# Kernel tuning notes

Hardware: AMD Instinct MI355X
Metric: run time of the kernel (lower is better)

Reference implementation:

```python
import jax, jax.numpy as jnp
import numpy as np

N_NODES = 100000
N_EDGES = 3200000
# (out_dim, in_dim) for the 4 BayesianLinear layers: mlp1 = [5->16, 16->32], mlp2 = [35->16, 16->1]
LAYER_DIMS = [(16, 5), (32, 16), (16, 35), (1, 16)]


def setup_inputs() -> dict:
    key = jax.random.key(0)
    ks = iter(jax.random.split(key, 32))
    inp = {}
    inp["x"] = jax.random.normal(next(ks), (N_NODES, 3), jnp.float32)
    inp["edge_attr"] = jax.random.normal(next(ks), (N_EDGES, 2), jnp.float32)
    inp["edge_index"] = jax.random.randint(next(ks), (2, N_EDGES), 0, N_NODES, dtype=jnp.int64)
    for li, (o, i) in enumerate(LAYER_DIMS, 1):
        inp[f"l{li}_wmu"] = jax.random.normal(next(ks), (o, i), jnp.float32) * 0.1
        inp[f"l{li}_wrho"] = jax.random.normal(next(ks), (o, i), jnp.float32) * 0.1 - 5.0
        inp[f"l{li}_bmu"] = jax.random.normal(next(ks), (o,), jnp.float32) * 0.1
        inp[f"l{li}_brho"] = jax.random.normal(next(ks), (o,), jnp.float32) * 0.1 - 5.0
        inp[f"l{li}_eps_w"] = jax.random.normal(next(ks), (o, i), jnp.float32)
        inp[f"l{li}_eps_b"] = jax.random.normal(next(ks), (o,), jnp.float32)
    return inp


def _bayes_linear(h, wmu, wrho, bmu, brho, eps_w, eps_b):
    # sampled weight: W = mu + softplus(rho) * eps  (blitz BayesianLinear)
    W = wmu + jax.nn.softplus(wrho) * eps_w          # [out, in]
    b = bmu + jax.nn.softplus(brho) * eps_b          # [out]
    return h @ W.T + b


def _igconv(x, edge_index, edge_attr, p1, p2, p3, p4):
    src, dst = edge_index[0], edge_index[1]          # x_j = x[src], aggregate at dst
    x_j = x[src]                                     # [E, 3] irregular gather
    m = jnp.concatenate([x_j, edge_attr], axis=1)    # [E, 5]
    m = jax.nn.relu(_bayes_linear(m, *p1))           # [E, 16]
    m = jax.nn.relu(_bayes_linear(m, *p2))           # [E, 32]
    agg = jax.ops.segment_max(m, dst, num_segments=x.shape[0])  # [N, 32]
    agg = jnp.where(jnp.isneginf(agg), 0.0, agg)     # nodes with no in-edges -> 0
    h = jnp.concatenate([x, agg], axis=1)            # [N, 35]
    h = jax.nn.relu(_bayes_linear(h, *p3))           # [N, 16]
    comb = jax.nn.sigmoid(_bayes_linear(h, *p4))     # [N, 1]
    return jnp.concatenate([x[:, :2], comb], axis=1) # [N, 3]


def reference(x, edge_attr, edge_index,
              l1_wmu, l1_wrho, l1_bmu, l1_brho, l1_eps_w, l1_eps_b,
              l2_wmu, l2_wrho, l2_bmu, l2_brho, l2_eps_w, l2_eps_b,
              l3_wmu, l3_wrho, l3_bmu, l3_brho, l3_eps_w, l3_eps_b,
              l4_wmu, l4_wrho, l4_bmu, l4_brho, l4_eps_w, l4_eps_b):
    p1 = (l1_wmu, l1_wrho, l1_bmu, l1_brho, l1_eps_w, l1_eps_b)
    p2 = (l2_wmu, l2_wrho, l2_bmu, l2_brho, l2_eps_w, l2_eps_b)
    p3 = (l3_wmu, l3_wrho, l3_bmu, l3_brho, l3_eps_w, l3_eps_b)
    p4 = (l4_wmu, l4_wrho, l4_bmu, l4_brho, l4_eps_w, l4_eps_b)
    h = x
    for _ in range(3):  # three stacked applications of the same IGConv
        h = _igconv(h, edge_index, edge_attr, p1, p2, p3, p4)
    return h
```

## Files before the change

kernel.cpp:

```cpp
#include <hip/hip_runtime.h>
#include <math.h>

#define WTOT  1233
#define PKOFS 1280
#define PKTOT 352

#define SCAT_CAP 12288

typedef __fp16 h2 __attribute__((ext_vector_type(2)));
typedef __fp16 f16x8 __attribute__((ext_vector_type(8)));
typedef float f32x16 __attribute__((ext_vector_type(16)));

__device__ __forceinline__ h2 u2h(unsigned int u) { return __builtin_bit_cast(h2, u); }
__device__ __forceinline__ unsigned int h2u(h2 h) { return __builtin_bit_cast(unsigned int, h); }
#define DOT2(a, b, c) __builtin_amdgcn_fdot2((a), (b), (c), false)

__device__ __forceinline__ float softplus_f(float x) {
  return fmaxf(x, 0.f) + log1pf(expf(-fabsf(x)));
}

struct PrepArgs {
  const float* wmu[4]; const float* wrho[4]; const float* epsw[4];
  const float* bmu[4]; const float* brho[4]; const float* epsb[4];
  float* out; int* bucketCur; int* etot; int nbuck;
};

__global__ void prep_all_kernel(PrepArgs a) {
  const int wsz[4] = {80, 512, 560, 16};
  const int wof[4] = {0, 96, 640, 1216};
  const int bsz[4] = {16, 32, 16, 1};
  const int bof[4] = {80, 608, 1200, 1232};
  float* wg = a.out;
  int tid = threadIdx.x;
  if (tid < a.nbuck) a.bucketCur[tid] = 0;
  if (tid == 1023) *a.etot = 0;
#pragma unroll
  for (int l = 0; l < 4; l++) {
    for (int i = tid; i < wsz[l]; i += 1024)
      wg[wof[l] + i] = a.wmu[l][i] + softplus_f(a.wrho[l][i]) * a.epsw[l][i];
    for (int i = tid; i < bsz[l]; i += 1024)
      wg[bof[l] + i] = a.bmu[l][i] + softplus_f(a.brho[l][i]) * a.epsb[l][i];
  }
  __syncthreads();
  unsigned int* wp = (unsigned int*)(wg + PKOFS);
  int t = tid;
  if (t < 16) {
    wp[t]      = h2u(h2{(__fp16)wg[t * 5 + 0], (__fp16)wg[t * 5 + 1]});
    wp[16 + t] = h2u(h2{(__fp16)wg[t * 5 + 2], (__fp16)0.f});
    wp[32 + t] = h2u(h2{(__fp16)wg[t * 5 + 3], (__fp16)wg[t * 5 + 4]});
    ((float*)wp)[304 + t] = wg[80 + t];
  }
  if (t < 32) {
    ((float*)wp)[320 + t] = wg[608 + t];
    for (int j = 0; j < 8; j++)
      wp[48 + t * 8 + j] =
          h2u(h2{(__fp16)wg[96 + t * 16 + 2 * j], (__fp16)wg[96 + t * 16 + 2 * j + 1]});
  }
}

__global__ __launch_bounds__(1024) void bhist_kernel(
    const int* __restrict__ dst, int* __restrict__ bucketCur,
    const float* __restrict__ x, uint2* __restrict__ xpk,
    unsigned int* __restrict__ agg32, int E, int N, int NBUCK) {
  __shared__ int h[1024];
  int tid = threadIdx.x;
  for (int i = tid; i < NBUCK; i += 1024) h[i] = 0;
  int nbase = blockIdx.x * 256;
  if (tid < 256) {
    int i = nbase + tid;
    if (i < N) {
      h2 a = __builtin_amdgcn_cvt_pkrtz(x[3 * i], x[3 * i + 1]);
      h2 b = __builtin_amdgcn_cvt_pkrtz(x[3 * i + 2], 0.f);
      xpk[i] = make_uint2(h2u(a), h2u(b));
    }
  }
  {
    uint4 z = make_uint4(0u, 0u, 0u, 0u);
    uint4* ap = (uint4*)agg32;
    size_t lim = ((size_t)N + 1) * 8;
    size_t i0 = (size_t)nbase * 8 + tid;
    if (i0 < lim) ap[i0] = z;
    size_t i1 = i0 + 1024;
    if (i1 < (size_t)(nbase + 256) * 8 && i1 < lim) ap[i1] = z;
  }
  __syncthreads();
  int base = blockIdx.x * 8192;
#pragma unroll
  for (int r = 0; r < 2; r++) {
    int e = base + r * 4096 + tid * 4;
    if (e + 3 < E) {
      int4 d4v = *(const int4*)(dst + e);
      atomicAdd(&h[d4v.x >> 8], 1);
      atomicAdd(&h[d4v.y >> 8], 1);
      atomicAdd(&h[d4v.z >> 8], 1);
      atomicAdd(&h[d4v.w >> 8], 1);
    } else {
      for (int k = 0; k < 4; k++)
        if (e + k < E) atomicAdd(&h[dst[e + k] >> 8], 1);
    }
  }
  __syncthreads();
  for (int i = tid; i < NBUCK; i += 1024) {
    int c = h[i];
    if (c) atomicAdd(&bucketCur[i], c);
  }
}

__global__ __launch_bounds__(1024) void scanBk_kernel(int* __restrict__ bucketCur,
                                                      int* __restrict__ bucketOff,
                                                      int NBUCK) {
  __shared__ int wsum[16];
  __shared__ int woff[16];
  int tid = threadIdx.x, lane = tid & 63, wid = tid >> 6;
  int v = (tid < NBUCK) ? bucketCur[tid] : 0;
  int x = v;
#pragma unroll
  for (int off = 1; off < 64; off <<= 1) {
    int t = __shfl_up(x, off, 64);
    if (lane >= off) x += t;
  }
  if (lane == 63) wsum[wid] = x;
  __syncthreads();
  if (wid == 0) {
    int s = (lane < 16) ? wsum[lane] : 0;
#pragma unroll
    for (int off = 1; off < 16; off <<= 1) {
      int t = __shfl_up(s, off, 64);
      if (lane >= off) s += t;
    }
    if (lane < 16) woff[lane] = s - wsum[lane];
  }
  __syncthreads();
  int excl = woff[wid] + x - v;
  if (tid < NBUCK) {
    bucketOff[tid] = excl;
    bucketCur[tid] = excl;
    if (tid == NBUCK - 1) bucketOff[NBUCK] = excl + v;
  }
}

__global__ __launch_bounds__(1024) void part_kernel(
    const int* __restrict__ src, const int* __restrict__ dst,
    const float2* __restrict__ ea, int* __restrict__ bucketCur,
    uint2* __restrict__ brec8, int E, int NBUCK) {
  __shared__ int h[1024];
  int tid = threadIdx.x;
  for (int i = tid; i < NBUCK; i += 1024) h[i] = 0;
  __syncthreads();
  int base = blockIdx.x * 8192;
  int d[8], s[8];
  unsigned int a[8];
  bool v[8];
#pragma unroll
  for (int j = 0; j < 8; j++) {
    int e = base + j * 1024 + tid;
    v[j] = e < E;
    if (v[j]) {
      d[j] = dst[e];
      s[j] = src[e];
      float2 t = ea[e];
      a[j] = h2u(__builtin_amdgcn_cvt_pkrtz(t.x, t.y));
      atomicAdd(&h[d[j] >> 8], 1);
    }
  }
  __syncthreads();
  for (int i = tid; i < NBUCK; i += 1024) {
    int c = h[i];
    h[i] = c ? atomicAdd(&bucketCur[i], c) : 0;
  }
  __syncthreads();
#pragma unroll
  for (int j = 0; j < 8; j++) {
    if (v[j]) {
      int pos = atomicAdd(&h[d[j] >> 8], 1);
      brec8[pos] = make_uint2(a[j], (unsigned int)s[j] | ((unsigned int)(d[j] & 255) << 24));
    }
  }
}

__global__ __launch_bounds__(1024) void scat_kernel(
    const uint2* __restrict__ brec8, const int* __restrict__ bucketOff,
    int* __restrict__ etot, uint2* __restrict__ se8, unsigned int* __restrict__ d4,
    int N) {
  __shared__ int cnt[256];
  __shared__ int sstart[256];
  __shared__ int wsum[4];
  __shared__ int woff[4];
  __shared__ int sbase;
  __shared__ int ptot;
  __shared__ __align__(16) uint2 stage[SCAT_CAP];
  __shared__ unsigned int staged4[SCAT_CAP / 4];
  int b = blockIdx.x, tid = threadIdx.x;
  int lane = tid & 63, wid = tid >> 6;
  if (tid < 256) cnt[tid] = 0;
  __syncthreads();
  int e0 = bucketOff[b], e1 = bucketOff[b + 1];
  for (int i = e0 + tid; i < e1; i += 1024) atomicAdd(&cnt[brec8[i].y >> 24], 1);
  __syncthreads();
  int v = 0;
  if (tid < 256) v = (cnt[tid] + 3) & ~3;
  int x = v;
#pragma unroll
  for (int off = 1; off < 64; off <<= 1) {
    int t = __shfl_up(x, off, 64);
    if (lane >= off) x += t;
  }
  if (tid < 256 && lane == 63) wsum[wid] = x;
  __syncthreads();
  if (wid == 0 && lane < 4) {
    int s = wsum[lane];
#pragma unroll
    for (int off = 1; off < 4; off <<= 1) {
      int t = __shfl_up(s, off, 64);
      if (lane >= off) s += t;
    }
    woff[lane] = s - wsum[lane];
    if (lane == 3) { ptot = s; sbase = atomicAdd(etot, s); }
  }
  __syncthreads();
  int total = ptot;
  if (total <= SCAT_CAP) {
    if (tid < 256) {
      int start = woff[wid] + x - v;
      sstart[tid] = start;
      cnt[tid] = start;
    }
    __syncthreads();
    for (int i = e0 + tid; i < e1; i += 1024) {
      uint2 t = brec8[i];
      int pos = atomicAdd(&cnt[t.y >> 24], 1);
      stage[pos] = make_uint2(t.y & 0x00FFFFFFu, t.x);
    }
    __syncthreads();
    if (tid < 256) {
      int start = sstart[tid];
      int endR = cnt[tid];
      int endP = start + ((endR - start + 3) & ~3);
      if (endR > start) {
        uint2 rep = stage[start];
        for (int k = endR; k < endP; k++) stage[k] = rep;
        unsigned int node = (unsigned int)(b * 256 + tid);
        for (int k = start; k < endP; k += 4) staged4[k >> 2] = node;
      }
    }
    __syncthreads();
    int base = sbase;
    uint4* dstp = (uint4*)(se8 + base);
    const uint4* srcp = (const uint4*)stage;
    int n4 = total >> 1;
    for (int i = tid; i < n4; i += 1024) dstp[i] = srcp[i];
    unsigned int* d4p = d4 + (base >> 2);
    int nd = total >> 2;
    for (int i = tid; i < nd; i += 1024) d4p[i] = staged4[i];
  } else {
    if (tid < 256) {
      int start = sbase + woff[wid] + x - v;
      sstart[tid] = start;
      cnt[tid] = start;
    }
    __syncthreads();
    for (int i = e0 + tid; i < e1; i += 1024) {
      uint2 t = brec8[i];
      int pos = atomicAdd(&cnt[t.y >> 24], 1);
      se8[pos] = make_uint2(t.y & 0x00FFFFFFu, t.x);
    }
    __syncthreads();
    if (tid < 256) {
      int node = b * 256 + tid;
      int start = sstart[tid];
      int endR = cnt[tid];
      int endP = start + ((endR - start + 3) & ~3);
      if (endR > start) {
        uint2 rep = se8[start];
        for (int k = endR; k < endP; k++) se8[k] = rep;
        for (int k = start; k < endP; k += 4) d4[k >> 2] = (unsigned int)node;
      }
    }
  }
}

__global__ __launch_bounds__(256) void edge_kernel(
    const uint2* __restrict__ xpk, const uint2* __restrict__ se8,
    const unsigned int* __restrict__ d4, unsigned int* __restrict__ agg32,
    const float* __restrict__ wg, const int* __restrict__ pEtot,
    unsigned int tag, int N) {
  __shared__ __align__(16) unsigned int lds[4][64][12];
  const unsigned int* wp = (const unsigned int*)(wg + PKOFS);
  const float* bf = (const float*)wp;
  const int Etot = *pEtot;
  if (blockIdx.x * 256 >= Etot) return;
  const int tid = threadIdx.x;
  const int lane = tid & 63;
  const int wslot = tid >> 6;
  const int e = blockIdx.x * 256 + tid;

  bool vld = e < Etot;
  uint2 se = vld ? se8[e] : make_uint2(0u, 0u);
  int d = vld ? (int)d4[e >> 2] : N;
  uint2 xs = xpk[se.x];

  h2 p01 = u2h(xs.x), p2v = u2h(xs.y), pea = u2h(se.y);
  unsigned int m1[8];
#pragma unroll
  for (int p = 0; p < 8; p++) {
    const int oA = 2 * p, oB = 2 * p + 1;
    float sA = DOT2(p01, u2h(wp[oA]),
                DOT2(p2v, u2h(wp[16 + oA]),
                DOT2(pea, u2h(wp[32 + oA]), bf[304 + oA])));
    float sB = DOT2(p01, u2h(wp[oB]),
                DOT2(p2v, u2h(wp[16 + oB]),
                DOT2(pea, u2h(wp[32 + oB]), bf[304 + oB])));
    m1[p] = h2u(__builtin_amdgcn_cvt_pkrtz(fmaxf(sA, 0.f), fmaxf(sB, 0.f)));
  }

  uint4* rowp = (uint4*)&lds[wslot][lane][0];
  rowp[0] = make_uint4(m1[0], m1[1], m1[2], m1[3]);
  rowp[1] = make_uint4(m1[4], m1[5], m1[6], m1[7]);
  asm volatile("s_waitcnt lgkmcnt(0)" ::: "memory");
  __builtin_amdgcn_sched_barrier(0);

  const int col = lane & 31;
  const int h = lane >> 5;
  f16x8 bfrag = __builtin_bit_cast(f16x8, *(const uint4*)&wp[48 + col * 8 + 4 * h]);
  float bias = bf[320 + col];
  f32x16 cini;
#pragma unroll
  for (int i = 0; i < 16; i++) cini[i] = bias;

  __builtin_amdgcn_s_setprio(1);
  f16x8 a0 = __builtin_bit_cast(f16x8, *(const uint4*)&lds[wslot][col][4 * h]);
  f16x8 a1 = __builtin_bit_cast(f16x8, *(const uint4*)&lds[wslot][32 + col][4 * h]);
  f32x16 acc0 = __builtin_amdgcn_mfma_f32_32x32x16_f16(a0, bfrag, cini, 0, 0, 0);
  f32x16 acc1 = __builtin_amdgcn_mfma_f32_32x32x16_f16(a1, bfrag, cini, 0, 0, 0);

  float bm[2][4];
#pragma unroll
  for (int q = 0; q < 4; q++) {
    bm[0][q] = fmaxf(fmaxf(acc0[4 * q], acc0[4 * q + 1]),
                     fmaxf(acc0[4 * q + 2], fmaxf(acc0[4 * q + 3], 0.f)));
    bm[1][q] = fmaxf(fmaxf(acc1[4 * q], acc1[4 * q + 1]),
                     fmaxf(acc1[4 * q + 2], fmaxf(acc1[4 * q + 3], 0.f)));
  }
  __builtin_amdgcn_s_setprio(0);

  int dp4 = __shfl_up(d, 4, 64);
  bool isHead = ((lane & 3) == 0) && (lane == 0 || d != dp4);
  unsigned long long hm = __ballot(isHead);

  unsigned long long rem = hm;
  while (rem) {
    int a = (int)__builtin_ctzll(rem);
    rem &= rem - 1;
    int b = rem ? (int)__builtin_ctzll(rem) : 64;
    int rd = __shfl(d, a, 64);
    int A = a >> 2, B = b >> 2;
    float mx = 0.f;
#pragma unroll
    for (int g = 0; g < 2; g++) {
#pragma unroll
      for (int q = 0; q < 4; q++) {
        int blk = 8 * g + 2 * q + h;
        bool in = (blk >= A) && (blk < B);
        mx = fmaxf(mx, in ? bm[g][q] : 0.f);
      }
    }
    mx = fmaxf(mx, __shfl_xor(mx, 32, 64));
    if (lane < 32 && rd < N) {
      unsigned int bits = __float_as_uint(mx);
      atomicMax(agg32 + (size_t)rd * 32 + col, (tag << 30) | (bits >> 1));
    }
  }
}

__global__ __launch_bounds__(256) void node_kernel(
    const float* __restrict__ x, const float* __restrict__ cin,
    float* __restrict__ cout, uint2* __restrict__ xpk,
    float* __restrict__ outFinal, const unsigned int* __restrict__ agg32,
    const float* __restrict__ wg, unsigned int tag, int n) {
  int nid = blockIdx.x * blockDim.x + threadIdx.x;
  if (nid >= n) return;
  const uint4* ap = (const uint4*)(agg32 + (size_t)nid * 32);
  uint4 q[8];
#pragma unroll
  for (int i = 0; i < 8; i++) q[i] = ap[i];
  float av[32];
#pragma unroll
  for (int i = 0; i < 8; i++) {
    unsigned int w[4] = {q[i].x, q[i].y, q[i].z, q[i].w};
#pragma unroll
    for (int j = 0; j < 4; j++) {
      unsigned int u = ((w[j] >> 30) == tag) ? ((w[j] & 0x3FFFFFFFu) << 1) : 0u;
      av[4 * i + j] = __uint_as_float(u);
    }
  }
  float x0 = x[3 * nid], x1 = x[3 * nid + 1];
  float x2 = cin ? cin[nid] : x[3 * nid + 2];
  float h[16];
#pragma unroll
  for (int o = 0; o < 16; o++) {
    float sa = wg[1200 + o];
    sa = fmaf(wg[640 + o * 35 + 0], x0, sa);
    sa = fmaf(wg[640 + o * 35 + 1], x1, sa);
    sa = fmaf(wg[640 + o * 35 + 2], x2, sa);
#pragma unroll
    for (int k = 0; k < 32; k++) sa = fmaf(wg[640 + o * 35 + 3 + k], av[k], sa);
    h[o] = fmaxf(sa, 0.f);
  }
  float z4 = wg[1232];
#pragma unroll
  for (int k = 0; k < 16; k++) z4 = fmaf(wg[1216 + k], h[k], z4);
  float comb = 1.f / (1.f + expf(-z4));
  cout[nid] = comb;
  ((unsigned int*)xpk)[2 * nid + 1] = h2u(__builtin_amdgcn_cvt_pkrtz(comb, 0.f));
  if (outFinal) {
    outFinal[3 * nid] = x0;
    outFinal[3 * nid + 1] = x1;
    outFinal[3 * nid + 2] = comb;
  }
}

extern "C" void kernel_launch(void* const* d_in, const int* in_sizes, int n_in,
                              void* d_out, int out_size, void* d_ws, size_t ws_size,
                              hipStream_t stream) {
  const float* x = (const float*)d_in[0];
  const float* ea = (const float*)d_in[1];
  const int* eidx = (const int*)d_in[2];
  const int N = in_sizes[0] / 3;
  const int E = in_sizes[1] / 2;
  const int* src = eidx;
  const int* dst = eidx + E;
  const int NBUCK = (N + 255) >> 8;
  const int EP = E + 3 * N;

  char* p = (char*)d_ws;
  size_t off = 0;
  auto alloc = [&](size_t bytes) -> char* {
    char* r = p + off;
    off = (off + bytes + 255) & ~(size_t)255;
    return r;
  };
  float* wbuf = (float*)alloc((size_t)(PKOFS + PKTOT) * 4);
  int* bucketOff = (int*)alloc(((size_t)NBUCK + 1) * 4);
  int* bucketCur = (int*)alloc((size_t)NBUCK * 4);
  int* etot = (int*)alloc(4);
  uint2* se8 = (uint2*)alloc((size_t)EP * 8);
  unsigned int* d4 = (unsigned int*)alloc(((size_t)(EP + 3) / 4 + 1) * 4);
  unsigned int* agg32 = (unsigned int*)alloc(((size_t)N + 1) * 32 * 4);
  uint2* xpk = (uint2*)alloc((size_t)N * 8);
  char* uni = alloc((size_t)E * 8);
  uint2* brec8 = (uint2*)uni;
  float* bufA = (float*)uni;
  float* bufB = (float*)(uni + (((size_t)N * 4 + 255) & ~(size_t)255));
  (void)ws_size;

  PrepArgs pa;
  for (int l = 0; l < 4; l++) {
    pa.wmu[l] = (const float*)d_in[3 + 6 * l + 0];
    pa.wrho[l] = (const float*)d_in[3 + 6 * l + 1];
    pa.bmu[l] = (const float*)d_in[3 + 6 * l + 2];
    pa.brho[l] = (const float*)d_in[3 + 6 * l + 3];
    pa.epsw[l] = (const float*)d_in[3 + 6 * l + 4];
    pa.epsb[l] = (const float*)d_in[3 + 6 * l + 5];
  }
  pa.out = wbuf;
  pa.bucketCur = bucketCur;
  pa.etot = etot;
  pa.nbuck = NBUCK;

  const int TB = 256;
  auto blocks = [&](int n) { return dim3((n + TB - 1) / TB); };

  prep_all_kernel<<<dim3(1), dim3(1024), 0, stream>>>(pa);
  {
    int gb = (E + 8191) / 8192;
    int gn = (N + 255) / 256;
    int g = gb > gn ? gb : gn;
    bhist_kernel<<<dim3(g), dim3(1024), 0, stream>>>(dst, bucketCur, x, xpk, agg32,
                                                     E, N, NBUCK);
  }
  scanBk_kernel<<<dim3(1), dim3(1024), 0, stream>>>(bucketCur, bucketOff, NBUCK);
  part_kernel<<<dim3((E + 8191) / 8192), dim3(1024), 0, stream>>>(
      src, dst, (const float2*)ea, bucketCur, brec8, E, NBUCK);
  scat_kernel<<<dim3(NBUCK), dim3(1024), 0, stream>>>(brec8, bucketOff, etot, se8, d4, N);

  float* outp = (float*)d_out;
  const int ebp = (EP + 255) / 256;
  edge_kernel<<<dim3(ebp), dim3(TB), 0, stream>>>(xpk, se8, d4, agg32, wbuf, etot, 1u, N);
  node_kernel<<<blocks(N), dim3(TB), 0, stream>>>(x, nullptr, bufA, xpk, nullptr,
                                                  agg32, wbuf, 1u, N);
  edge_kernel<<<dim3(ebp), dim3(TB), 0, stream>>>(xpk, se8, d4, agg32, wbuf, etot, 2u, N);
  node_kernel<<<blocks(N), dim3(TB), 0, stream>>>(x, bufA, bufB, xpk, nullptr,
                                                  agg32, wbuf, 2u, N);
  edge_kernel<<<dim3(ebp), dim3(TB), 0, stream>>>(xpk, se8, d4, agg32, wbuf, etot, 3u, N);
  node_kernel<<<blocks(N), dim3(TB), 0, stream>>>(x, bufB, bufA, xpk, outp,
                                                  agg32, wbuf, 3u, N);
}
```

Measured before the change: 326.4 us.

## Make edge kernel persistent grid-stride per wave with prefetch of next edge tile

Caps the edge kernel grid at 2048 blocks and has each wave loop over 64-edge tiles in a grid-stride fashion. While it processes the current tile it prefetches the next tile's sorted edge records and destination indices. Per-wave setup such as the B fragment and bias is loaded once and reused across tiles. This aims to cut launch and block overhead and hide load latency, at the cost of extra registers and possibly less latency hiding from oversubscription.

```diff
diff --git a/kernel.cpp b/kernel.cpp
--- a/kernel.cpp
+++ b/kernel.cpp
@@ -266,14 +266,14 @@
     }
     __syncthreads();
     if (tid < 256) {
-      int node = b * 256 + tid;
+      unsigned int node = (unsigned int)(b * 256 + tid);
       int start = sstart[tid];
       int endR = cnt[tid];
       int endP = start + ((endR - start + 3) & ~3);
       if (endR > start) {
         uint2 rep = se8[start];
         for (int k = endR; k < endP; k++) se8[k] = rep;
-        for (int k = start; k < endP; k += 4) d4[k >> 2] = (unsigned int)node;
+        for (int k = start; k < endP; k += 4) d4[k >> 2] = node;
       }
     }
   }
@@ -283,41 +283,16 @@
     const uint2* __restrict__ xpk, const uint2* __restrict__ se8,
     const unsigned int* __restrict__ d4, unsigned int* __restrict__ agg32,
     const float* __restrict__ wg, const int* __restrict__ pEtot,
-    unsigned int tag, int N) {
+    unsigned int tag, int N, int nwv) {
   __shared__ __align__(16) unsigned int lds[4][64][12];
   const unsigned int* wp = (const unsigned int*)(wg + PKOFS);
   const float* bf = (const float*)wp;
   const int Etot = *pEtot;
-  if (blockIdx.x * 256 >= Etot) return;
   const int tid = threadIdx.x;
   const int lane = tid & 63;
   const int wslot = tid >> 6;
-  const int e = blockIdx.x * 256 + tid;
-
-  bool vld = e < Etot;
-  uint2 se = vld ? se8[e] : make_uint2(0u, 0u);
-  int d = vld ? (int)d4[e >> 2] : N;
-  uint2 xs = xpk[se.x];
-
-  h2 p01 = u2h(xs.x), p2v = u2h(xs.y), pea = u2h(se.y);
-  unsigned int m1[8];
-#pragma unroll
-  for (int p = 0; p < 8; p++) {
-    const int oA = 2 * p, oB = 2 * p + 1;
-    float sA = DOT2(p01, u2h(wp[oA]),
-                DOT2(p2v, u2h(wp[16 + oA]),
-                DOT2(pea, u2h(wp[32 + oA]), bf[304 + oA])));
-    float sB = DOT2(p01, u2h(wp[oB]),
-                DOT2(p2v, u2h(wp[16 + oB]),
-                DOT2(pea, u2h(wp[32 + oB]), bf[304 + oB])));
-    m1[p] = h2u(__builtin_amdgcn_cvt_pkrtz(fmaxf(sA, 0.f), fmaxf(sB, 0.f)));
-  }
-
-  uint4* rowp = (uint4*)&lds[wslot][lane][0];
-  rowp[0] = make_uint4(m1[0], m1[1], m1[2], m1[3]);
-  rowp[1] = make_uint4(m1[4], m1[5], m1[6], m1[7]);
-  asm volatile("s_waitcnt lgkmcnt(0)" ::: "memory");
-  __builtin_amdgcn_sched_barrier(0);
+  int w = blockIdx.x * 4 + wslot;
+  if (w * 64 >= Etot) return;
 
   const int col = lane & 31;
   const int h = lane >> 5;
@@ -327,48 +302,93 @@
 #pragma unroll
   for (int i = 0; i < 16; i++) cini[i] = bias;
 
-  __builtin_amdgcn_s_setprio(1);
-  f16x8 a0 = __builtin_bit_cast(f16x8, *(const uint4*)&lds[wslot][col][4 * h]);
-  f16x8 a1 = __builtin_bit_cast(f16x8, *(const uint4*)&lds[wslot][32 + col][4 * h]);
-  f32x16 acc0 = __builtin_amdgcn_mfma_f32_32x32x16_f16(a0, bfrag, cini, 0, 0, 0);
-  f32x16 acc1 = __builtin_amdgcn_mfma_f32_32x32x16_f16(a1, bfrag, cini, 0, 0, 0);
-
-  float bm[2][4];
-#pragma unroll
-  for (int q = 0; q < 4; q++) {
-    bm[0][q] = fmaxf(fmaxf(acc0[4 * q], acc0[4 * q + 1]),
-                     fmaxf(acc0[4 * q + 2], fmaxf(acc0[4 * q + 3], 0.f)));
-    bm[1][q] = fmaxf(fmaxf(acc1[4 * q], acc1[4 * q + 1]),
-                     fmaxf(acc1[4 * q + 2], fmaxf(acc1[4 * q + 3], 0.f)));
-  }
-  __builtin_amdgcn_s_setprio(0);
-
-  int dp4 = __shfl_up(d, 4, 64);
-  bool isHead = ((lane & 3) == 0) && (lane == 0 || d != dp4);
-  unsigned long long hm = __ballot(isHead);
-
-  unsigned long long rem = hm;
-  while (rem) {
-    int a = (int)__builtin_ctzll(rem);
-    rem &= rem - 1;
-    int b = rem ? (int)__builtin_ctzll(rem) : 64;
-    int rd = __shfl(d, a, 64);
-    int A = a >> 2, B = b >> 2;
-    float mx = 0.f;
-#pragma unroll
-    for (int g = 0; g < 2; g++) {
-#pragma unroll
-      for (int q = 0; q < 4; q++) {
-        int blk = 8 * g + 2 * q + h;
-        bool in = (blk >= A) && (blk < B);
-        mx = fmaxf(mx, in ? bm[g][q] : 0.f);
+  int e = w * 64 + lane;
+  uint2 seC = (e < Etot) ? se8[e] : make_uint2(0u, 0u);
+  int dC = (e < Etot) ? (int)d4[e >> 2] : N;
+
+  while (true) {
+    int wn = w + nwv;
+    bool hasNext = (wn * 64 < Etot);
+    uint2 seN = make_uint2(0u, 0u);
+    int dN = N;
+    if (hasNext) {
+      int en = wn * 64 + lane;
+      if (en < Etot) {
+        seN = se8[en];
+        dN = (int)d4[en >> 2];
       }
     }
-    mx = fmaxf(mx, __shfl_xor(mx, 32, 64));
-    if (lane < 32 && rd < N) {
-      unsigned int bits = __float_as_uint(mx);
-      atomicMax(agg32 + (size_t)rd * 32 + col, (tag << 30) | (bits >> 1));
-    }
+
+    uint2 xs = xpk[seC.x];
+    h2 p01 = u2h(xs.x), p2v = u2h(xs.y), pea = u2h(seC.y);
+    unsigned int m1[8];
+#pragma unroll
+    for (int p = 0; p < 8; p++) {
+      const int oA = 2 * p, oB = 2 * p + 1;
+      float sA = DOT2(p01, u2h(wp[oA]),
+                  DOT2(p2v, u2h(wp[16 + oA]),
+                  DOT2(pea, u2h(wp[32 + oA]), bf[304 + oA])));
+      float sB = DOT2(p01, u2h(wp[oB]),
+                  DOT2(p2v, u2h(wp[16 + oB]),
+                  DOT2(pea, u2h(wp[32 + oB]), bf[304 + oB])));
+      m1[p] = h2u(__builtin_amdgcn_cvt_pkrtz(fmaxf(sA, 0.f), fmaxf(sB, 0.f)));
+    }
+
+    uint4* rowp = (uint4*)&lds[wslot][lane][0];
+    rowp[0] = make_uint4(m1[0], m1[1], m1[2], m1[3]);
+    rowp[1] = make_uint4(m1[4], m1[5], m1[6], m1[7]);
+    asm volatile("s_waitcnt lgkmcnt(0)" ::: "memory");
+    __builtin_amdgcn_sched_barrier(0);
+
+    __builtin_amdgcn_s_setprio(1);
+    f16x8 a0 = __builtin_bit_cast(f16x8, *(const uint4*)&lds[wslot][col][4 * h]);
+    f16x8 a1 = __builtin_bit_cast(f16x8, *(const uint4*)&lds[wslot][32 + col][4 * h]);
+    f32x16 acc0 = __builtin_amdgcn_mfma_f32_32x32x16_f16(a0, bfrag, cini, 0, 0, 0);
+    f32x16 acc1 = __builtin_amdgcn_mfma_f32_32x32x16_f16(a1, bfrag, cini, 0, 0, 0);
+
+    float bm[2][4];
+#pragma unroll
+    for (int q = 0; q < 4; q++) {
+      bm[0][q] = fmaxf(fmaxf(acc0[4 * q], acc0[4 * q + 1]),
+                       fmaxf(acc0[4 * q + 2], fmaxf(acc0[4 * q + 3], 0.f)));
+      bm[1][q] = fmaxf(fmaxf(acc1[4 * q], acc1[4 * q + 1]),
+                       fmaxf(acc1[4 * q + 2], fmaxf(acc1[4 * q + 3], 0.f)));
+    }
+    __builtin_amdgcn_s_setprio(0);
+
+    int d = dC;
+    int dp4 = __shfl_up(d, 4, 64);
+    bool isHead = ((lane & 3) == 0) && (lane == 0 || d != dp4);
+    unsigned long long hm = __ballot(isHead);
+
+    unsigned long long rem = hm;
+    while (rem) {
+      int a = (int)__builtin_ctzll(rem);
+      rem &= rem - 1;
+      int b = rem ? (int)__builtin_ctzll(rem) : 64;
+      int rd = __shfl(d, a, 64);
+      int A = a >> 2, B = b >> 2;
+      float mx = 0.f;
+#pragma unroll
+      for (int g = 0; g < 2; g++) {
+#pragma unroll
+        for (int q = 0; q < 4; q++) {
+          int blk = 8 * g + 2 * q + h;
+          bool in = (blk >= A) && (blk < B);
+          mx = fmaxf(mx, in ? bm[g][q] : 0.f);
+        }
+      }
+      mx = fmaxf(mx, __shfl_xor(mx, 32, 64));
+      if (lane < 32 && rd < N) {
+        unsigned int bits = __float_as_uint(mx);
+        atomicMax(agg32 + (size_t)rd * 32 + col, (tag << 30) | (bits >> 1));
+      }
+    }
+
+    if (!hasNext) break;
+    w = wn;
+    seC = seN;
+    dC = dN;
   }
 }
 
@@ -484,14 +504,19 @@
   scat_kernel<<<dim3(NBUCK), dim3(1024), 0, stream>>>(brec8, bucketOff, etot, se8, d4, N);
 
   float* outp = (float*)d_out;
-  const int ebp = (EP + 255) / 256;
-  edge_kernel<<<dim3(ebp), dim3(TB), 0, stream>>>(xpk, se8, d4, agg32, wbuf, etot, 1u, N);
+  int ebp = (EP + 255) / 256;
+  if (ebp > 2048) ebp = 2048;
+  const int nwv = ebp * 4;
+  edge_kernel<<<dim3(ebp), dim3(TB), 0, stream>>>(xpk, se8, d4, agg32, wbuf, etot,
+                                                  1u, N, nwv);
   node_kernel<<<blocks(N), dim3(TB), 0, stream>>>(x, nullptr, bufA, xpk, nullptr,
                                                   agg32, wbuf, 1u, N);
-  edge_kernel<<<dim3(ebp), dim3(TB), 0, stream>>>(xpk, se8, d4, agg32, wbuf, etot, 2u, N);
+  edge_kernel<<<dim3(ebp), dim3(TB), 0, stream>>>(xpk, se8, d4, agg32, wbuf, etot,
+                                                  2u, N, nwv);
   node_kernel<<<blocks(N), dim3(TB), 0, stream>>>(x, bufA, bufB, xpk, nullptr,
                                                   agg32, wbuf, 2u, N);
-  edge_kernel<<<dim3(ebp), dim3(TB), 0, stream>>>(xpk, se8, d4, agg32, wbuf, etot, 3u, N);
+  edge_kernel<<<dim3(ebp), dim3(TB), 0, stream>>>(xpk, se8, d4, agg32, wbuf, etot,
+                                                  3u, N, nwv);
   node_kernel<<<blocks(N), dim3(TB), 0, stream>>>(x, bufB, bufA, xpk, outp,
                                                   agg32, wbuf, 3u, N);
 }
```

Result: slower. 333.1 us (+2.0%).
